# Performance work log

Hardware: AMD Instinct MI355X
Metric: run time of the kernel (lower is better)

The kernel has to match this reference:

```python
import jax, jax.numpy as jnp
import numpy as np

N = 100000          # num nodes
NUM_GRAPHS = 64
NEG_SLOPE = 0.2     # PyG GATv2Conv default


def gatv2_layer(x, src, dst, Wl, bl, Wr, br, att, bias, heads, out_ch, concat):
    # x: [N, F_in]; src/dst: [E] (self-loops already included)
    xl = (x @ Wl + bl).reshape(-1, heads, out_ch)   # source transform
    xr = (x @ Wr + br).reshape(-1, heads, out_ch)   # target transform
    m = jax.nn.leaky_relu(xl[src] + xr[dst], NEG_SLOPE)      # [E, H, C]
    alpha = jnp.einsum('ehc,hc->eh', m, att)                 # [E, H]
    # segment softmax over destination nodes
    amax = jax.ops.segment_max(alpha, dst, num_segments=N)
    alpha = jnp.exp(alpha - amax[dst])
    denom = jax.ops.segment_sum(alpha, dst, num_segments=N)
    alpha = alpha / (denom[dst] + 1e-16)
    out = jax.ops.segment_sum(xl[src] * alpha[..., None], dst, num_segments=N)
    out = out.reshape(N, heads * out_ch) if concat else out.mean(axis=1)
    return out + bias


def setup_inputs() -> dict:
    key = jax.random.key(0)
    ks = jax.random.split(key, 16)
    E = 3200000
    x = jax.random.normal(ks[0], (N, 256), dtype=jnp.float32)
    edge_index = jax.random.randint(ks[1], (2, E), 0, N, dtype=jnp.int64)
    batch = jnp.sort(jax.random.randint(ks[2], (N,), 0, NUM_GRAPHS, dtype=jnp.int64))
    H1, C1 = 8, 4
    s1 = 1.0 / np.sqrt(256)
    s2 = 1.0 / np.sqrt(H1 * C1)
    return {
        'x': x, 'edge_index': edge_index, 'batch': batch,
        'W1l': jax.random.normal(ks[3], (256, H1 * C1), jnp.float32) * s1,
        'b1l': jnp.zeros((H1 * C1,), jnp.float32),
        'W1r': jax.random.normal(ks[4], (256, H1 * C1), jnp.float32) * s1,
        'b1r': jnp.zeros((H1 * C1,), jnp.float32),
        'att1': jax.random.normal(ks[5], (H1, C1), jnp.float32),
        'bias1': jnp.zeros((H1 * C1,), jnp.float32),
        'W2l': jax.random.normal(ks[6], (H1 * C1, 64), jnp.float32) * s2,
        'b2l': jnp.zeros((64,), jnp.float32),
        'W2r': jax.random.normal(ks[7], (H1 * C1, 64), jnp.float32) * s2,
        'b2r': jnp.zeros((64,), jnp.float32),
        'att2': jax.random.normal(ks[8], (1, 64), jnp.float32),
        'bias2': jnp.zeros((64,), jnp.float32),
    }


def reference(x, edge_index, batch, W1l, b1l, W1r, b1r, att1, bias1,
              W2l, b2l, W2r, b2r, att2, bias2):
    # add self-loops (PyG GATv2Conv default add_self_loops=True)
    loop = jnp.arange(N, dtype=edge_index.dtype)
    src = jnp.concatenate([edge_index[0], loop])
    dst = jnp.concatenate([edge_index[1], loop])
    h = gatv2_layer(x, src, dst, W1l, b1l, W1r, b1r, att1, bias1, 8, 4, True)
    h = jax.nn.elu(h)
    h = gatv2_layer(h, src, dst, W2l, b2l, W2r, b2r, att2, bias2, 1, 64, False)
    # global mean pool over graphs
    sums = jax.ops.segment_sum(h, batch, num_segments=NUM_GRAPHS)
    counts = jax.ops.segment_sum(jnp.ones((N, 1), h.dtype), batch, num_segments=NUM_GRAPHS)
    return sums / jnp.maximum(counts, 1.0)
```

## Files before the change

kernel.cpp:

```cpp
#include <hip/hip_runtime.h>
#include <math.h>

#define NN 100000
#define EE 3200000
#define ET (EE + NN)
#define NG 64

#define NB 196
#define BWID 512
#define PCHUNK 8192
#define PBLOCKS ((ET + PCHUNK - 1) / PCHUNK)

#define X1_SPLIT 50048
#define X1BLK_A 391
#define X1BLK_B 391

#define OFF_XL1B  0u
#define OFF_XR1   1600000u
#define OFF_H     4800000u
#define OFF_HL2B  8000000u
#define OFF_HR2   11200000u
#define OFF_BEDGE 8000000u
#define OFF_RP    17600000u
#define OFF_ESRC  17700096u
#define OFF_POOL  21000096u
#define OFF_CNTG  21004192u
#define OFF_BCNT  21004256u
#define OFF_BOFF  21004512u
#define OFF_GCUR  21004768u
#define WS_UNITS  21005024u

__device__ __forceinline__ float lrelu(float v) { return v > 0.0f ? v : 0.2f * v; }

__device__ __forceinline__ unsigned pack_bf2(float a, float b) {
  unsigned ua = __float_as_uint(a), ub = __float_as_uint(b);
  ua = (ua + 0x7FFFu + ((ua >> 16) & 1u)) >> 16;
  ub = (ub + 0x7FFFu + ((ub >> 16) & 1u)) & 0xFFFF0000u;
  return ua | ub;
}
__device__ __forceinline__ float bf_lo(unsigned u) { return __uint_as_float(u << 16); }
__device__ __forceinline__ float bf_hi(unsigned u) { return __uint_as_float(u & 0xFFFF0000u); }

__global__ __launch_bounds__(256) void k_bcount(const int* __restrict__ ei,
                                                int* __restrict__ bcnt) {
  __shared__ int h[NB];
  for (int i = threadIdx.x; i < NB; i += 256) h[i] = 0;
  __syncthreads();
  for (long e = (long)blockIdx.x * 256 + threadIdx.x; e < ET; e += (long)gridDim.x * 256) {
    int d = (e < EE) ? ei[EE + e] : (int)(e - EE);
    atomicAdd(&h[d >> 9], 1);
  }
  __syncthreads();
  for (int i = threadIdx.x; i < NB; i += 256) if (h[i]) atomicAdd(&bcnt[i], h[i]);
}

__global__ __launch_bounds__(256) void k_bscan(const int* __restrict__ bcnt,
                                               int* __restrict__ boff, int* __restrict__ gcur) {
  __shared__ int sd[256];
  int t = threadIdx.x;
  int v = (t < NB) ? bcnt[t] : 0;
  sd[t] = v;
  __syncthreads();
  for (int o = 1; o < 256; o <<= 1) {
    int u = (t >= o) ? sd[t - o] : 0;
    __syncthreads();
    sd[t] += u;
    __syncthreads();
  }
  if (t < NB) { boff[t] = sd[t] - v; gcur[t] = sd[t] - v; }
  if (t == 0) boff[NB] = ET;
}

__device__ void part_role(char* smem, const int* __restrict__ ei,
                          int* __restrict__ gcur, int* __restrict__ bedge, int pblk) {
  int* cnt   = (int*)smem;
  int* lbase = cnt + NB;
  int* gbase = lbase + NB;
  int* sc    = gbase + NB;
  int* buf   = sc + 256;
  unsigned char* bkt = (unsigned char*)(buf + PCHUNK);
  int tid = threadIdx.x;
  long e0 = (long)pblk * PCHUNK;
  int nedge = (e0 + PCHUNK <= ET) ? PCHUNK : (int)(ET - e0);

  for (int i = tid; i < NB; i += 512) cnt[i] = 0;
  __syncthreads();
  for (int i = tid; i < nedge; i += 512) {
    long e = e0 + i;
    int d = (e < EE) ? ei[EE + e] : (int)(e - EE);
    atomicAdd(&cnt[d >> 9], 1);
  }
  __syncthreads();
  if (tid < 256) sc[tid] = (tid < NB) ? cnt[tid] : 0;
  __syncthreads();
  for (int o = 1; o < 256; o <<= 1) {
    int u = (tid < 256 && tid >= o) ? sc[tid - o] : 0;
    __syncthreads();
    if (tid < 256) sc[tid] += u;
    __syncthreads();
  }
  if (tid < NB) lbase[tid] = sc[tid] - cnt[tid];
  __syncthreads();
  if (tid < NB) {
    int c = cnt[tid];
    gbase[tid] = c ? atomicAdd(&gcur[tid], c) : 0;
    cnt[tid] = 0;
  }
  __syncthreads();
  for (int i = tid; i < nedge; i += 512) {
    long e = e0 + i;
    int s, d;
    if (e < EE) { s = ei[e]; d = ei[EE + e]; }
    else { s = (int)(e - EE); d = s; }
    int b = d >> 9;
    int r = atomicAdd(&cnt[b], 1);
    int idx = lbase[b] + r;
    buf[idx] = s | ((d & 511) << 17);
    bkt[idx] = (unsigned char)b;
  }
  __syncthreads();
  for (int i = tid; i < nedge; i += 512) {
    int p = buf[i];
    int b = bkt[i];
    bedge[gbase[b] + (i - lbase[b])] = p;
  }
}

__device__ void csr_role(char* smem, const int* __restrict__ boff,
                         const int* __restrict__ bedge,
                         int* __restrict__ rp, int* __restrict__ esrc, int b) {
  int* sdeg  = (int*)smem;
  int* sscan = sdeg + BWID;
  int t = threadIdx.x;
  int n0 = b * BWID;
  int lo = boff[b], hi = boff[b + 1];
  sdeg[t] = 0;
  __syncthreads();
  for (int i = lo + t; i < hi; i += 512) {
    int p = bedge[i];
    atomicAdd(&sdeg[p >> 17], 1);
  }
  __syncthreads();
  int v = sdeg[t];
  sscan[t] = v;
  __syncthreads();
  for (int o = 1; o < 512; o <<= 1) {
    int u = (t >= o) ? sscan[t - o] : 0;
    __syncthreads();
    sscan[t] += u;
    __syncthreads();
  }
  int excl = sscan[t] - v;
  int n = n0 + t;
  if (n < NN) rp[n] = lo + excl;
  if (b == NB - 1 && t == 0) rp[NN] = ET;
  __syncthreads();
  sdeg[t] = lo + excl;
  __syncthreads();
  for (int i = lo + t; i < hi; i += 512) {
    int p = bedge[i];
    int pos = atomicAdd(&sdeg[p >> 17], 1);
    esrc[pos] = p & 0x1FFFF;
  }
}

#define FMA4A(a, xv) \
  a.x += xv.x*w0.x + xv.y*w1.x + xv.z*w2.x + xv.w*w3.x; \
  a.y += xv.x*w0.y + xv.y*w1.y + xv.z*w2.y + xv.w*w3.y; \
  a.z += xv.x*w0.z + xv.y*w1.z + xv.z*w2.z + xv.w*w3.z; \
  a.w += xv.x*w0.w + xv.y*w1.w + xv.z*w2.w + xv.w*w3.w;

__device__ void xform1_role(char* smem, const float* __restrict__ x,
                            const float* __restrict__ Wl, const float* __restrict__ bl,
                            const float* __restrict__ Wr, const float* __restrict__ br,
                            unsigned short* __restrict__ xl1b, float* __restrict__ xr1,
                            int n_base) {
  float* Wlds = (float*)smem;
  int tid = threadIdx.x;
  int ci = tid & 15;
  int cbase = ci * 4;
  int n0 = n_base + (tid >> 4) * 4;
  int r0 = n0 + 0 < NN ? n0 + 0 : NN - 1;
  int r1 = n0 + 1 < NN ? n0 + 1 : NN - 1;
  int r2 = n0 + 2 < NN ? n0 + 2 : NN - 1;
  int r3 = n0 + 3 < NN ? n0 + 3 : NN - 1;
  const float* xb0 = x + (size_t)r0 * 256;
  const float* xb1 = x + (size_t)r1 * 256;
  const float* xb2 = x + (size_t)r2 * 256;
  const float* xb3 = x + (size_t)r3 * 256;
  float4 acc0 = {0,0,0,0}, acc1 = {0,0,0,0}, acc2 = {0,0,0,0}, acc3 = {0,0,0,0};

  for (int q = 0; q < 4; ++q) {
    int k0 = q * 64;
    __syncthreads();
    for (int i = tid; i < 64 * 64; i += 512) {
      int k = (i >> 6) + k0, c = i & 63;
      Wlds[i] = (c < 32) ? Wl[k * 32 + c] : Wr[k * 32 + (c - 32)];
    }
    __syncthreads();
#pragma unroll 2
    for (int kk = 0; kk < 64; kk += 4) {
      int k = k0 + kk;
      float4 xv0 = *(const float4*)(xb0 + k);
      float4 xv1 = *(const float4*)(xb1 + k);
      float4 xv2 = *(const float4*)(xb2 + k);
      float4 xv3 = *(const float4*)(xb3 + k);
      const float* wr = &Wlds[kk * 64 + cbase];
      float4 w0 = *(const float4*)(wr);
      float4 w1 = *(const float4*)(wr + 64);
      float4 w2 = *(const float4*)(wr + 128);
      float4 w3 = *(const float4*)(wr + 192);
      FMA4A(acc0, xv0)
      FMA4A(acc1, xv1)
      FMA4A(acc2, xv2)
      FMA4A(acc3, xv3)
    }
  }
  float4 acc[4] = {acc0, acc1, acc2, acc3};
  if (cbase < 32) {
    float4 bv = { bl[cbase], bl[cbase+1], bl[cbase+2], bl[cbase+3] };
#pragma unroll
    for (int j = 0; j < 4; ++j) {
      int n = n0 + j;
      if (n < NN) {
        uint2 o = { pack_bf2(acc[j].x + bv.x, acc[j].y + bv.y),
                    pack_bf2(acc[j].z + bv.z, acc[j].w + bv.w) };
        *(uint2*)(xl1b + (size_t)n * 32 + cbase) = o;
      }
    }
  } else {
    int c2 = cbase - 32;
    float4 bv = { br[c2], br[c2+1], br[c2+2], br[c2+3] };
#pragma unroll
    for (int j = 0; j < 4; ++j) {
      int n = n0 + j;
      if (n < NN) {
        float4 o = { acc[j].x + bv.x, acc[j].y + bv.y, acc[j].z + bv.z, acc[j].w + bv.w };
        *(float4*)(xr1 + (size_t)n * 32 + c2) = o;
      }
    }
  }
}

__global__ __launch_bounds__(512) void k_part_x1(
    const int* __restrict__ ei, int* __restrict__ gcur, int* __restrict__ bedge,
    const float* __restrict__ x,
    const float* __restrict__ Wl, const float* __restrict__ bl,
    const float* __restrict__ Wr, const float* __restrict__ br,
    unsigned short* __restrict__ xl1b, float* __restrict__ xr1) {
  extern __shared__ char smem[];
  if (blockIdx.x < PBLOCKS)
    part_role(smem, ei, gcur, bedge, blockIdx.x);
  else
    xform1_role(smem, x, Wl, bl, Wr, br, xl1b, xr1, (blockIdx.x - PBLOCKS) * 128);
}

__global__ __launch_bounds__(512) void k_csr_x1(
    const int* __restrict__ boff, const int* __restrict__ bedge,
    int* __restrict__ rp, int* __restrict__ esrc,
    const float* __restrict__ x,
    const float* __restrict__ Wl, const float* __restrict__ bl,
    const float* __restrict__ Wr, const float* __restrict__ br,
    unsigned short* __restrict__ xl1b, float* __restrict__ xr1) {
  extern __shared__ char smem[];
  if (blockIdx.x < NB)
    csr_role(smem, boff, bedge, rp, esrc, blockIdx.x);
  else
    xform1_role(smem, x, Wl, bl, Wr, br, xl1b, xr1,
                X1_SPLIT + (blockIdx.x - NB) * 128);
}

__global__ __launch_bounds__(256) void k_gather1(
    const int* __restrict__ rp, const int* __restrict__ esrc,
    const unsigned short* __restrict__ xl1b, const float* __restrict__ xr1,
    const float* __restrict__ att1, const float* __restrict__ bias1,
    float* __restrict__ h) {
  int n = blockIdx.x * 8 + (threadIdx.x >> 5);
  if (n >= NN) return;
  int l = threadIdx.x & 31;
  float av = att1[l];
  float xr = xr1[(size_t)n * 32 + l];
  int rpn = rp[n], dg = rp[n + 1] - rpn;
  float acc = 0.0f, den = 0.0f;
  int j = 0;
  for (; j + 4 <= dg; j += 4) {
    int s0 = esrc[rpn + j + 0];
    int s1 = esrc[rpn + j + 1];
    int s2 = esrc[rpn + j + 2];
    int s3 = esrc[rpn + j + 3];
    float x0 = bf_lo(xl1b[(size_t)s0 * 32 + l]);
    float x1 = bf_lo(xl1b[(size_t)s1 * 32 + l]);
    float x2 = bf_lo(xl1b[(size_t)s2 * 32 + l]);
    float x3 = bf_lo(xl1b[(size_t)s3 * 32 + l]);
    float p0 = lrelu(x0 + xr) * av;
    float p1 = lrelu(x1 + xr) * av;
    float p2 = lrelu(x2 + xr) * av;
    float p3 = lrelu(x3 + xr) * av;
    p0 += __shfl_xor(p0, 1); p1 += __shfl_xor(p1, 1);
    p2 += __shfl_xor(p2, 1); p3 += __shfl_xor(p3, 1);
    p0 += __shfl_xor(p0, 2); p1 += __shfl_xor(p1, 2);
    p2 += __shfl_xor(p2, 2); p3 += __shfl_xor(p3, 2);
    float w0 = __expf(p0), w1 = __expf(p1), w2 = __expf(p2), w3 = __expf(p3);
    den += w0 + w1 + w2 + w3;
    acc += w0 * x0 + w1 * x1 + w2 * x2 + w3 * x3;
  }
  for (; j < dg; ++j) {
    int s = esrc[rpn + j];
    float xl = bf_lo(xl1b[(size_t)s * 32 + l]);
    float p = lrelu(xl + xr) * av;
    p += __shfl_xor(p, 1);
    p += __shfl_xor(p, 2);
    float w = __expf(p);
    den += w;
    acc += w * xl;
  }
  float v = acc / (den + 1e-16f) + bias1[l];
  h[(size_t)n * 32 + l] = v > 0.0f ? v : expm1f(v);
}

__global__ __launch_bounds__(256) void k_xform2(
    const float* __restrict__ h,
    const float* __restrict__ Wl, const float* __restrict__ bl,
    const float* __restrict__ Wr, const float* __restrict__ br,
    unsigned short* __restrict__ hl2b, float* __restrict__ hr2) {
  __shared__ float Wlds[32 * 128];
  int tid = threadIdx.x;
  for (int i = tid; i < 32 * 128; i += 256) {
    int k = i >> 7, c = i & 127;
    Wlds[i] = (c < 64) ? Wl[k * 64 + c] : Wr[k * 64 + (c - 64)];
  }
  __syncthreads();
  int ci = tid & 31, ni = tid >> 5;
  int cbase = ci * 4;
  int n0 = blockIdx.x * 32 + ni * 4;
  const float* hb0 = h + (size_t)(n0 + 0) * 32;
  const float* hb1 = h + (size_t)(n0 + 1) * 32;
  const float* hb2 = h + (size_t)(n0 + 2) * 32;
  const float* hb3 = h + (size_t)(n0 + 3) * 32;
  float4 acc0 = {0,0,0,0}, acc1 = {0,0,0,0}, acc2 = {0,0,0,0}, acc3 = {0,0,0,0};
#pragma unroll
  for (int k = 0; k < 32; k += 4) {
    float4 xv0 = *(const float4*)(hb0 + k);
    float4 xv1 = *(const float4*)(hb1 + k);
    float4 xv2 = *(const float4*)(hb2 + k);
    float4 xv3 = *(const float4*)(hb3 + k);
    const float* wr = &Wlds[k * 128 + cbase];
    float4 w0 = *(const float4*)(wr);
    float4 w1 = *(const float4*)(wr + 128);
    float4 w2 = *(const float4*)(wr + 256);
    float4 w3 = *(const float4*)(wr + 384);
    FMA4A(acc0, xv0)
    FMA4A(acc1, xv1)
    FMA4A(acc2, xv2)
    FMA4A(acc3, xv3)
  }
  float4 acc[4] = {acc0, acc1, acc2, acc3};
  if (cbase < 64) {
    float4 bv = { bl[cbase], bl[cbase+1], bl[cbase+2], bl[cbase+3] };
#pragma unroll
    for (int j = 0; j < 4; ++j) {
      uint2 o = { pack_bf2(acc[j].x + bv.x, acc[j].y + bv.y),
                  pack_bf2(acc[j].z + bv.z, acc[j].w + bv.w) };
      *(uint2*)(hl2b + (size_t)(n0 + j) * 64 + cbase) = o;
    }
  } else {
    int c2 = cbase - 64;
    float4 bv = { br[c2], br[c2+1], br[c2+2], br[c2+3] };
#pragma unroll
    for (int j = 0; j < 4; ++j) {
      float4 o = { acc[j].x + bv.x, acc[j].y + bv.y, acc[j].z + bv.z, acc[j].w + bv.w };
      *(float4*)(hr2 + (size_t)(n0 + j) * 64 + c2) = o;
    }
  }
}

#define G2_P(qq, pp) { \
  float4 U0 = { bf_lo(qq.x), bf_hi(qq.x), bf_lo(qq.y), bf_hi(qq.y) }; \
  float4 U1 = { bf_lo(qq.z), bf_hi(qq.z), bf_lo(qq.w), bf_hi(qq.w) }; \
  pp = lrelu(U0.x + hr0.x) * ac0.x + lrelu(U0.y + hr0.y) * ac0.y \
     + lrelu(U0.z + hr0.z) * ac0.z + lrelu(U0.w + hr0.w) * ac0.w \
     + lrelu(U1.x + hr1.x) * ac1.x + lrelu(U1.y + hr1.y) * ac1.y \
     + lrelu(U1.z + hr1.z) * ac1.z + lrelu(U1.w + hr1.w) * ac1.w; }

#define G2_ACC(qq, ww) { \
  float4 U0 = { bf_lo(qq.x), bf_hi(qq.x), bf_lo(qq.y), bf_hi(qq.y) }; \
  float4 U1 = { bf_lo(qq.z), bf_hi(qq.z), bf_lo(qq.w), bf_hi(qq.w) }; \
  a0.x += ww * U0.x; a0.y += ww * U0.y; a0.z += ww * U0.z; a0.w += ww * U0.w; \
  a1.x += ww * U1.x; a1.y += ww * U1.y; a1.z += ww * U1.z; a1.w += ww * U1.w; }

__global__ __launch_bounds__(256) void k_gather2(
    const int* __restrict__ rp, const int* __restrict__ esrc,
    const unsigned short* __restrict__ hl2b, const float* __restrict__ hr2,
    const float* __restrict__ att2, const float* __restrict__ bias2,
    const int* __restrict__ batch,
    float* __restrict__ pool, float* __restrict__ cntg) {
  __shared__ float ssum[4][64];
  __shared__ float scnt[4];
  int tid = threadIdx.x;
  int n = (blockIdx.x * 256 + tid) >> 3;
  int l8 = tid & 7;
  int nblk0 = blockIdx.x * 32;
  int gmin = batch[nblk0];
  int gspan = batch[nblk0 + 31] - gmin + 1;
  ssum[tid >> 6][tid & 63] = 0.0f;
  if (tid < 4) scnt[tid] = 0.0f;
  __syncthreads();

  float4 ac0 = *(const float4*)(att2 + l8 * 8);
  float4 ac1 = *(const float4*)(att2 + l8 * 8 + 4);
  float4 bs0 = *(const float4*)(bias2 + l8 * 8);
  float4 bs1 = *(const float4*)(bias2 + l8 * 8 + 4);
  const float4* hrp = (const float4*)(hr2 + (size_t)n * 64 + l8 * 8);
  float4 hr0 = hrp[0], hr1 = hrp[1];
  int rpn = rp[n], dg = rp[n + 1] - rpn;
  float4 a0 = {0,0,0,0}, a1 = {0,0,0,0};
  float den = 0.0f;
  int j = 0;
  for (; j + 4 <= dg; j += 4) {
    int s0 = esrc[rpn + j + 0];
    int s1 = esrc[rpn + j + 1];
    int s2 = esrc[rpn + j + 2];
    int s3 = esrc[rpn + j + 3];
    uint4 q0 = *(const uint4*)(hl2b + (size_t)s0 * 64 + l8 * 8);
    uint4 q1 = *(const uint4*)(hl2b + (size_t)s1 * 64 + l8 * 8);
    uint4 q2 = *(const uint4*)(hl2b + (size_t)s2 * 64 + l8 * 8);
    uint4 q3 = *(const uint4*)(hl2b + (size_t)s3 * 64 + l8 * 8);
    float p0, p1, p2, p3;
    G2_P(q0, p0) G2_P(q1, p1) G2_P(q2, p2) G2_P(q3, p3)
    p0 += __shfl_xor(p0, 1); p1 += __shfl_xor(p1, 1);
    p2 += __shfl_xor(p2, 1); p3 += __shfl_xor(p3, 1);
    p0 += __shfl_xor(p0, 2); p1 += __shfl_xor(p1, 2);
    p2 += __shfl_xor(p2, 2); p3 += __shfl_xor(p3, 2);
    p0 += __shfl_xor(p0, 4); p1 += __shfl_xor(p1, 4);
    p2 += __shfl_xor(p2, 4); p3 += __shfl_xor(p3, 4);
    float w0 = __expf(p0), w1 = __expf(p1), w2 = __expf(p2), w3 = __expf(p3);
    den += w0 + w1 + w2 + w3;
    G2_ACC(q0, w0) G2_ACC(q1, w1) G2_ACC(q2, w2) G2_ACC(q3, w3)
  }
  for (; j < dg; ++j) {
    int s = esrc[rpn + j];
    uint4 q0 = *(const uint4*)(hl2b + (size_t)s * 64 + l8 * 8);
    float p;
    G2_P(q0, p)
    p += __shfl_xor(p, 1);
    p += __shfl_xor(p, 2);
    p += __shfl_xor(p, 4);
    float w = __expf(p);
    den += w;
    G2_ACC(q0, w)
  }
  float inv = 1.0f / (den + 1e-16f);
  int gi = batch[n] - gmin;
  float* sp = &ssum[gi][l8 * 8];
  atomicAdd(sp + 0, a0.x * inv + bs0.x);
  atomicAdd(sp + 1, a0.y * inv + bs0.y);
  atomicAdd(sp + 2, a0.z * inv + bs0.z);
  atomicAdd(sp + 3, a0.w * inv + bs0.w);
  atomicAdd(sp + 4, a1.x * inv + bs1.x);
  atomicAdd(sp + 5, a1.y * inv + bs1.y);
  atomicAdd(sp + 6, a1.z * inv + bs1.z);
  atomicAdd(sp + 7, a1.w * inv + bs1.w);
  if (l8 == 0) atomicAdd(&scnt[gi], 1.0f);
  __syncthreads();
  for (int i = tid; i < gspan * 64; i += 256)
    atomicAdd(pool + (size_t)(gmin + (i >> 6)) * 64 + (i & 63), ssum[i >> 6][i & 63]);
  if (tid < gspan) atomicAdd(cntg + gmin + tid, scnt[tid]);
}

__global__ __launch_bounds__(256) void k_final(
    const float* __restrict__ pool, const float* __restrict__ cntg,
    float* __restrict__ out) {
  int i = blockIdx.x * 256 + threadIdx.x;
  if (i < NG * 64) out[i] = pool[i] / fmaxf(cntg[i >> 6], 1.0f);
}

extern "C" void kernel_launch(void* const* d_in, const int* in_sizes, int n_in,
                              void* d_out, int out_size, void* d_ws, size_t ws_size,
                              hipStream_t stream) {
  const float* x     = (const float*)d_in[0];
  const int*   ei    = (const int*)d_in[1];
  const int*   batch = (const int*)d_in[2];
  const float* W1l   = (const float*)d_in[3];
  const float* b1l   = (const float*)d_in[4];
  const float* W1r   = (const float*)d_in[5];
  const float* b1r   = (const float*)d_in[6];
  const float* att1  = (const float*)d_in[7];
  const float* bias1 = (const float*)d_in[8];
  const float* W2l   = (const float*)d_in[9];
  const float* b2l   = (const float*)d_in[10];
  const float* W2r   = (const float*)d_in[11];
  const float* b2r   = (const float*)d_in[12];
  const float* att2  = (const float*)d_in[13];
  const float* bias2 = (const float*)d_in[14];
  float* ws = (float*)d_ws;
  int*   wi = (int*)d_ws;
  float* out = (float*)d_out;

  hipMemsetAsync(ws + OFF_POOL, 0, (size_t)(WS_UNITS - OFF_POOL) * 4, stream);

  k_bcount<<<512, 256, 0, stream>>>(ei, wi + OFF_BCNT);
  k_bscan<<<1, 256, 0, stream>>>(wi + OFF_BCNT, wi + OFF_BOFF, wi + OFF_GCUR);
  k_part_x1<<<PBLOCKS + X1BLK_A, 512, 44352, stream>>>(
      ei, wi + OFF_GCUR, wi + OFF_BEDGE,
      x, W1l, b1l, W1r, b1r, (unsigned short*)(ws + OFF_XL1B), ws + OFF_XR1);
  k_csr_x1<<<NB + X1BLK_B, 512, 16384, stream>>>(
      wi + OFF_BOFF, wi + OFF_BEDGE, wi + OFF_RP, wi + OFF_ESRC,
      x, W1l, b1l, W1r, b1r, (unsigned short*)(ws + OFF_XL1B), ws + OFF_XR1);

  k_gather1<<<NN / 8, 256, 0, stream>>>(wi + OFF_RP, wi + OFF_ESRC,
                                        (const unsigned short*)(ws + OFF_XL1B), ws + OFF_XR1,
                                        att1, bias1, ws + OFF_H);
  k_xform2<<<NN / 32, 256, 0, stream>>>(ws + OFF_H, W2l, b2l, W2r, b2r,
                                        (unsigned short*)(ws + OFF_HL2B), ws + OFF_HR2);
  k_gather2<<<(NN * 8 + 255) / 256, 256, 0, stream>>>(wi + OFF_RP, wi + OFF_ESRC,
                                                      (const unsigned short*)(ws + OFF_HL2B),
                                                      ws + OFF_HR2, att2, bias2, batch,
                                                      ws + OFF_POOL, ws + OFF_CNTG);
  k_final<<<16, 256, 0, stream>>>(ws + OFF_POOL, ws + OFF_CNTG, out);
}
```

Baseline: 355.7 us.

## Fuse layer-1 gather with layer-2 transform and unroll gather2 by eight

Merges the layer-1 attention gather and the layer-2 linear transform into one kernel: each block computes the ELU outputs of eight nodes into shared memory and immediately multiplies them by the layer-2 weights staged in LDS. This removes the intermediate h buffer write/read and one kernel launch. The layer-2 gather loop is unrolled to eight edges per iteration for more loads in flight, and leaky-ReLU becomes an fmax. In exchange, every 8-node block now reloads the full 32x128 weight matrix into LDS (12500 blocks versus 3125 before), and the larger unroll raises register pressure.

```diff
diff --git a/kernel.cpp b/kernel.cpp
--- a/kernel.cpp
+++ b/kernel.cpp
@@ -17,7 +17,6 @@
 
 #define OFF_XL1B  0u
 #define OFF_XR1   1600000u
-#define OFF_H     4800000u
 #define OFF_HL2B  8000000u
 #define OFF_HR2   11200000u
 #define OFF_BEDGE 8000000u
@@ -30,7 +29,7 @@
 #define OFF_GCUR  21004768u
 #define WS_UNITS  21005024u
 
-__device__ __forceinline__ float lrelu(float v) { return v > 0.0f ? v : 0.2f * v; }
+__device__ __forceinline__ float lrelu(float v) { return fmaxf(v, 0.2f * v); }
 
 __device__ __forceinline__ unsigned pack_bf2(float a, float b) {
   unsigned ua = __float_as_uint(a), ub = __float_as_uint(b);
@@ -270,14 +269,22 @@
                 X1_SPLIT + (blockIdx.x - NB) * 128);
 }
 
-__global__ __launch_bounds__(256) void k_gather1(
+__global__ __launch_bounds__(256) void k_gather1x2(
     const int* __restrict__ rp, const int* __restrict__ esrc,
     const unsigned short* __restrict__ xl1b, const float* __restrict__ xr1,
     const float* __restrict__ att1, const float* __restrict__ bias1,
-    float* __restrict__ h) {
-  int n = blockIdx.x * 8 + (threadIdx.x >> 5);
-  if (n >= NN) return;
-  int l = threadIdx.x & 31;
+    const float* __restrict__ W2l, const float* __restrict__ b2l,
+    const float* __restrict__ W2r, const float* __restrict__ b2r,
+    unsigned short* __restrict__ hl2b, float* __restrict__ hr2) {
+  __shared__ float W2lds[32 * 128];
+  __shared__ float hlds[8][33];
+  int tid = threadIdx.x;
+  for (int i = tid; i < 32 * 128; i += 256) {
+    int k = i >> 7, c = i & 127;
+    W2lds[i] = (c < 64) ? W2l[k * 64 + c] : W2r[k * 64 + (c - 64)];
+  }
+  int n = blockIdx.x * 8 + (tid >> 5);
+  int l = tid & 31;
   float av = att1[l];
   float xr = xr1[(size_t)n * 32 + l];
   int rpn = rp[n], dg = rp[n + 1] - rpn;
@@ -315,62 +322,27 @@
     acc += w * xl;
   }
   float v = acc / (den + 1e-16f) + bias1[l];
-  h[(size_t)n * 32 + l] = v > 0.0f ? v : expm1f(v);
-}
-
-__global__ __launch_bounds__(256) void k_xform2(
-    const float* __restrict__ h,
-    const float* __restrict__ Wl, const float* __restrict__ bl,
-    const float* __restrict__ Wr, const float* __restrict__ br,
-    unsigned short* __restrict__ hl2b, float* __restrict__ hr2) {
-  __shared__ float Wlds[32 * 128];
-  int tid = threadIdx.x;
-  for (int i = tid; i < 32 * 128; i += 256) {
-    int k = i >> 7, c = i & 127;
-    Wlds[i] = (c < 64) ? Wl[k * 64 + c] : Wr[k * 64 + (c - 64)];
-  }
-  __syncthreads();
-  int ci = tid & 31, ni = tid >> 5;
-  int cbase = ci * 4;
-  int n0 = blockIdx.x * 32 + ni * 4;
-  const float* hb0 = h + (size_t)(n0 + 0) * 32;
-  const float* hb1 = h + (size_t)(n0 + 1) * 32;
-  const float* hb2 = h + (size_t)(n0 + 2) * 32;
-  const float* hb3 = h + (size_t)(n0 + 3) * 32;
-  float4 acc0 = {0,0,0,0}, acc1 = {0,0,0,0}, acc2 = {0,0,0,0}, acc3 = {0,0,0,0};
-#pragma unroll
-  for (int k = 0; k < 32; k += 4) {
-    float4 xv0 = *(const float4*)(hb0 + k);
-    float4 xv1 = *(const float4*)(hb1 + k);
-    float4 xv2 = *(const float4*)(hb2 + k);
-    float4 xv3 = *(const float4*)(hb3 + k);
-    const float* wr = &Wlds[k * 128 + cbase];
-    float4 w0 = *(const float4*)(wr);
-    float4 w1 = *(const float4*)(wr + 128);
-    float4 w2 = *(const float4*)(wr + 256);
-    float4 w3 = *(const float4*)(wr + 384);
-    FMA4A(acc0, xv0)
-    FMA4A(acc1, xv1)
-    FMA4A(acc2, xv2)
-    FMA4A(acc3, xv3)
-  }
-  float4 acc[4] = {acc0, acc1, acc2, acc3};
+  v = v > 0.0f ? v : expm1f(v);
+  hlds[tid >> 5][l] = v;
+  __syncthreads();
+
+  int ni = tid >> 5, ci = tid & 31, cbase = ci * 4;
+  float4 a = {0,0,0,0};
+#pragma unroll
+  for (int k = 0; k < 32; ++k) {
+    float hv = hlds[ni][k];
+    float4 wv = *(const float4*)(&W2lds[k * 128 + cbase]);
+    a.x += hv * wv.x; a.y += hv * wv.y; a.z += hv * wv.z; a.w += hv * wv.w;
+  }
+  int no = blockIdx.x * 8 + ni;
   if (cbase < 64) {
-    float4 bv = { bl[cbase], bl[cbase+1], bl[cbase+2], bl[cbase+3] };
-#pragma unroll
-    for (int j = 0; j < 4; ++j) {
-      uint2 o = { pack_bf2(acc[j].x + bv.x, acc[j].y + bv.y),
-                  pack_bf2(acc[j].z + bv.z, acc[j].w + bv.w) };
-      *(uint2*)(hl2b + (size_t)(n0 + j) * 64 + cbase) = o;
-    }
+    uint2 o = { pack_bf2(a.x + b2l[cbase], a.y + b2l[cbase + 1]),
+                pack_bf2(a.z + b2l[cbase + 2], a.w + b2l[cbase + 3]) };
+    *(uint2*)(hl2b + (size_t)no * 64 + cbase) = o;
   } else {
     int c2 = cbase - 64;
-    float4 bv = { br[c2], br[c2+1], br[c2+2], br[c2+3] };
-#pragma unroll
-    for (int j = 0; j < 4; ++j) {
-      float4 o = { acc[j].x + bv.x, acc[j].y + bv.y, acc[j].z + bv.z, acc[j].w + bv.w };
-      *(float4*)(hr2 + (size_t)(n0 + j) * 64 + c2) = o;
-    }
+    float4 o = { a.x + b2r[c2], a.y + b2r[c2 + 1], a.z + b2r[c2 + 2], a.w + b2r[c2 + 3] };
+    *(float4*)(hr2 + (size_t)no * 64 + c2) = o;
   }
 }
 
@@ -416,26 +388,28 @@
   float4 a0 = {0,0,0,0}, a1 = {0,0,0,0};
   float den = 0.0f;
   int j = 0;
-  for (; j + 4 <= dg; j += 4) {
-    int s0 = esrc[rpn + j + 0];
-    int s1 = esrc[rpn + j + 1];
-    int s2 = esrc[rpn + j + 2];
-    int s3 = esrc[rpn + j + 3];
-    uint4 q0 = *(const uint4*)(hl2b + (size_t)s0 * 64 + l8 * 8);
-    uint4 q1 = *(const uint4*)(hl2b + (size_t)s1 * 64 + l8 * 8);
-    uint4 q2 = *(const uint4*)(hl2b + (size_t)s2 * 64 + l8 * 8);
-    uint4 q3 = *(const uint4*)(hl2b + (size_t)s3 * 64 + l8 * 8);
-    float p0, p1, p2, p3;
-    G2_P(q0, p0) G2_P(q1, p1) G2_P(q2, p2) G2_P(q3, p3)
-    p0 += __shfl_xor(p0, 1); p1 += __shfl_xor(p1, 1);
-    p2 += __shfl_xor(p2, 1); p3 += __shfl_xor(p3, 1);
-    p0 += __shfl_xor(p0, 2); p1 += __shfl_xor(p1, 2);
-    p2 += __shfl_xor(p2, 2); p3 += __shfl_xor(p3, 2);
-    p0 += __shfl_xor(p0, 4); p1 += __shfl_xor(p1, 4);
-    p2 += __shfl_xor(p2, 4); p3 += __shfl_xor(p3, 4);
-    float w0 = __expf(p0), w1 = __expf(p1), w2 = __expf(p2), w3 = __expf(p3);
-    den += w0 + w1 + w2 + w3;
-    G2_ACC(q0, w0) G2_ACC(q1, w1) G2_ACC(q2, w2) G2_ACC(q3, w3)
+  for (; j + 8 <= dg; j += 8) {
+    int s[8];
+#pragma unroll
+    for (int t = 0; t < 8; ++t) s[t] = esrc[rpn + j + t];
+    uint4 q[8];
+#pragma unroll
+    for (int t = 0; t < 8; ++t) q[t] = *(const uint4*)(hl2b + (size_t)s[t] * 64 + l8 * 8);
+    float p[8];
+#pragma unroll
+    for (int t = 0; t < 8; ++t) { G2_P(q[t], p[t]) }
+#pragma unroll
+    for (int t = 0; t < 8; ++t) {
+      p[t] += __shfl_xor(p[t], 1);
+      p[t] += __shfl_xor(p[t], 2);
+      p[t] += __shfl_xor(p[t], 4);
+    }
+#pragma unroll
+    for (int t = 0; t < 8; ++t) {
+      float w = __expf(p[t]);
+      den += w;
+      G2_ACC(q[t], w)
+    }
   }
   for (; j < dg; ++j) {
     int s = esrc[rpn + j];
@@ -507,11 +481,10 @@
       wi + OFF_BOFF, wi + OFF_BEDGE, wi + OFF_RP, wi + OFF_ESRC,
       x, W1l, b1l, W1r, b1r, (unsigned short*)(ws + OFF_XL1B), ws + OFF_XR1);
 
-  k_gather1<<<NN / 8, 256, 0, stream>>>(wi + OFF_RP, wi + OFF_ESRC,
-                                        (const unsigned short*)(ws + OFF_XL1B), ws + OFF_XR1,
-                                        att1, bias1, ws + OFF_H);
-  k_xform2<<<NN / 32, 256, 0, stream>>>(ws + OFF_H, W2l, b2l, W2r, b2r,
-                                        (unsigned short*)(ws + OFF_HL2B), ws + OFF_HR2);
+  k_gather1x2<<<NN / 8, 256, 0, stream>>>(wi + OFF_RP, wi + OFF_ESRC,
+                                          (const unsigned short*)(ws + OFF_XL1B), ws + OFF_XR1,
+                                          att1, bias1, W2l, b2l, W2r, b2r,
+                                          (unsigned short*)(ws + OFF_HL2B), ws + OFF_HR2);
   k_gather2<<<(NN * 8 + 255) / 256, 256, 0, stream>>>(wi + OFF_RP, wi + OFF_ESRC,
                                                       (const unsigned short*)(ws + OFF_HL2B),
                                                       ws + OFF_HR2, att2, bias2, batch,
```

Result: no change. 359.8 us (+1.1%).
